# Kernel optimization log

Measured on AMD Instinct MI355X. Metric: run time of the kernel, lower is better.

The kernel has to match this reference:

```python
import jax, jax.numpy as jnp
import numpy as np

N, E, ND, ED, HID = 50000, 400000, 128, 64, 128
GIN = 2 * ND + 2  # gnn1 input dim
CIN = 2 * HID + ED  # classifier input dim


def seg_mean(v, idx, n):
    s = jax.ops.segment_sum(v, idx, num_segments=n)
    cnt = jax.ops.segment_sum(jnp.ones((v.shape[0], 1), v.dtype), idx, num_segments=n)
    return s / jnp.maximum(cnt, 1.0)


def layer_norm(h, g, b):
    mu = h.mean(-1, keepdims=True)
    var = ((h - mu) ** 2).mean(-1, keepdims=True)
    return (h - mu) / jnp.sqrt(var + 1e-5) * g + b


def gatv2(h, src, dst, ea, wl, wr, we, att, bias, n, heads):
    # PyG GATv2Conv, concat=False, negative_slope=0.2, add_self_loops with fill_value='mean'
    C = wl.shape[1] // heads
    loop_attr = seg_mean(ea, dst, n)  # self-loop edge_attr = mean of incoming edge_attr
    ar = jnp.arange(n, dtype=src.dtype)
    s = jnp.concatenate([src, ar])
    d = jnp.concatenate([dst, ar])
    ea2 = jnp.concatenate([ea, loop_attr], axis=0)
    xl = (h @ wl).reshape(n, heads, C)
    xr = (h @ wr).reshape(n, heads, C)
    e = xl[s] + xr[d] + (ea2 @ we).reshape(-1, heads, C)  # [E2, H, C]
    e = jax.nn.leaky_relu(e, 0.2)
    logit = (e * att).sum(-1)  # [E2, H]
    m = jax.ops.segment_max(logit, d, num_segments=n)
    m = jnp.where(jnp.isfinite(m), m, 0.0)
    a = jnp.exp(logit - m[d])
    denom = jax.ops.segment_sum(a, d, num_segments=n)
    a = a / jnp.maximum(denom[d], 1e-16)
    out = jax.ops.segment_sum(xl[s] * a[..., None], d, num_segments=n)  # [N, H, C]
    return out.mean(axis=1) + bias


def setup_inputs() -> dict:
    key = jax.random.key(0)
    ks = jax.random.split(key, 32)
    w = lambda k, sh: jax.random.normal(k, sh, jnp.float32) * 0.05
    x = jax.random.normal(ks[0], (N, ND), jnp.float32)
    node_stats = jax.random.uniform(ks[1], (N, 2), jnp.float32)
    src = jax.random.randint(ks[2], (E,), 0, N)
    dst = (src + 1 + jax.random.randint(ks[3], (E,), 0, N - 1)) % N  # guarantees src != dst
    edge_index = jnp.stack([src, dst]).astype(jnp.int32)
    edge_attr = jax.random.normal(ks[4], (E, ED), jnp.float32)
    return {
        'x': x, 'node_stats': node_stats, 'edge_index': edge_index, 'edge_attr': edge_attr,
        'epw': w(ks[5], (ED, ND)), 'epb': jnp.zeros((ND,), jnp.float32),
        'g1wl': w(ks[6], (GIN, 2 * HID)), 'g1wr': w(ks[7], (GIN, 2 * HID)),
        'g1we': w(ks[8], (ED, 2 * HID)), 'g1att': w(ks[9], (2, HID)), 'g1b': jnp.zeros((HID,), jnp.float32),
        'n1g': jnp.ones((HID,), jnp.float32), 'n1b': jnp.zeros((HID,), jnp.float32),
        'g2wl': w(ks[10], (HID, HID)), 'g2wr': w(ks[11], (HID, HID)),
        'g2we': w(ks[12], (ED, HID)), 'g2att': w(ks[13], (1, HID)), 'g2b': jnp.zeros((HID,), jnp.float32),
        'n2g': jnp.ones((HID,), jnp.float32), 'n2b': jnp.zeros((HID,), jnp.float32),
        'c1w': w(ks[14], (CIN, HID)), 'c1b': jnp.zeros((HID,), jnp.float32),
        'c2w': w(ks[15], (HID, HID // 2)), 'c2b': jnp.zeros((HID // 2,), jnp.float32),
        'c3w': w(ks[16], (HID // 2, 1)), 'c3b': jnp.zeros((1,), jnp.float32),
    }


def reference(x, node_stats, edge_index, edge_attr, epw, epb, g1wl, g1wr, g1we, g1att, g1b,
              n1g, n1b, g2wl, g2wr, g2we, g2att, g2b, n2g, n2b, c1w, c1b, c2w, c2b, c3w, c3b):
    src, dst = edge_index[0], edge_index[1]
    n = x.shape[0]
    emb = jax.nn.relu(edge_attr @ epw + epb)  # [E, ND]
    x_out = seg_mean(emb, src, n)
    x_in = seg_mean(emb, dst, n)
    xi = jnp.concatenate([x_out, x_in, node_stats], axis=1)  # [N, GIN]
    h1 = jax.nn.elu(layer_norm(gatv2(xi, src, dst, edge_attr, g1wl, g1wr, g1we, g1att, g1b, n, 2), n1g, n1b))
    h2 = jax.nn.elu(layer_norm(gatv2(h1, src, dst, edge_attr, g2wl, g2wr, g2we, g2att, g2b, n, 1), n2g, n2b))
    er = jnp.concatenate([h2[src], h2[dst], edge_attr], axis=1)  # [E, CIN]
    h = jax.nn.relu(er @ c1w + c1b)
    h = jax.nn.relu(h @ c2w + c2b)
    return h @ c3w + c3b  # [E, 1]
```

## Files before the change

kernel.cpp:

```cpp
#include <hip/hip_runtime.h>
#include <cstdint>
#include <cstddef>


static inline int cdiv(int a, int b) { return (a + b - 1) / b; }

typedef __attribute__((ext_vector_type(8))) short bfrag;
typedef __attribute__((ext_vector_type(4))) float ffrag;

__device__ __forceinline__ float bf2f(unsigned short u) {
  return __uint_as_float(((unsigned)u) << 16);
}
__device__ __forceinline__ unsigned short f2bf(float f) {
  unsigned b = __float_as_uint(f);
  return (unsigned short)((b + 0x7FFFu + ((b >> 16) & 1u)) >> 16);
}

struct PrepJobs {
  const float* src[11];
  unsigned short* dst[11];
  int K[11], Nc[11], KC[11], ld[11];
};
__global__ void prep_bt(PrepJobs J) {
  int j = blockIdx.x;
  int K = J.K[j], Nc = J.Nc[j], KC = J.KC[j], ld = J.ld[j];
  const float* S = J.src[j];
  unsigned short* D = J.dst[j];
  for (int n = blockIdx.y; n < Nc; n += gridDim.y)
    for (int t = threadIdx.x; t < KC; t += blockDim.x) {
      float v = (t < K) ? S[(size_t)t * ld + n] : 0.f;
      D[(size_t)n * KC + t] = f2bf(v);
    }
}

__global__ __launch_bounds__(256) void cvt_bf16(const float* __restrict__ in,
                                                unsigned short* __restrict__ out,
                                                int n4) {
  for (int i = blockIdx.x * blockDim.x + threadIdx.x; i < n4;
       i += gridDim.x * blockDim.x) {
    float4 v = ((const float4*)in)[i];
    ((ushort4*)out)[i] = make_ushort4(f2bf(v.x), f2bf(v.y), f2bf(v.z), f2bf(v.w));
  }
}

__global__ void count_deg(const int* __restrict__ src, const int* __restrict__ dst,
                          int* __restrict__ dsrc, int* __restrict__ ddst, int E) {
  int t = blockIdx.x * blockDim.x + threadIdx.x;
  if (t < E) {
    atomicAdd(&dsrc[src[t]], 1);
    atomicAdd(&ddst[dst[t]], 1);
  }
}

__global__ __launch_bounds__(256) void scan_local(
    const int* __restrict__ degA, const int* __restrict__ degB,
    int* __restrict__ rowA, int* __restrict__ rowB, int* __restrict__ bsum,
    int N, int nb) {
  __shared__ int s[256];
  int arr = blockIdx.y;
  const int* deg = arr ? degB : degA;
  int* row = arr ? rowB : rowA;
  int b = blockIdx.x;
  int i = b * 256 + threadIdx.x;
  int v = (i < N) ? deg[i] : 0;
  s[threadIdx.x] = v;
  __syncthreads();
  for (int off = 1; off < 256; off <<= 1) {
    int t = (threadIdx.x >= off) ? s[threadIdx.x - off] : 0;
    __syncthreads();
    s[threadIdx.x] += t;
    __syncthreads();
  }
  int incl = s[threadIdx.x];
  if (i < N) row[i] = incl - v;
  if (threadIdx.x == 255) bsum[arr * nb + b] = incl;
}

__global__ __launch_bounds__(1024) void scan_bsums(int* __restrict__ bsum, int nb,
                                                   int* __restrict__ rowA,
                                                   int* __restrict__ rowB, int N) {
  __shared__ int s[1024];
  int tid = threadIdx.x;
  for (int arr = 0; arr < 2; arr++) {
    int v = (tid < nb) ? bsum[arr * nb + tid] : 0;
    s[tid] = v;
    __syncthreads();
    for (int off = 1; off < 1024; off <<= 1) {
      int t = (tid >= off) ? s[tid - off] : 0;
      __syncthreads();
      s[tid] += t;
      __syncthreads();
    }
    if (tid < nb) bsum[arr * nb + tid] = s[tid] - v;
    if (tid == nb - 1) {
      int* row = arr ? rowB : rowA;
      row[N] = s[tid];
    }
    __syncthreads();
  }
}

__global__ void scan_add(int* __restrict__ rowA, int* __restrict__ rowB,
                         int* __restrict__ curA, const int* __restrict__ bsum,
                         int N, int nb) {
  int arr = blockIdx.y;
  int* row = arr ? rowB : rowA;
  int b = blockIdx.x;
  int i = b * 256 + threadIdx.x;
  if (i < N) {
    int v = row[i] + bsum[arr * nb + b];
    row[i] = v;
    if (arr == 0) curA[i] = v;
  }
}

__global__ void ext_fix(const int* __restrict__ row_dst, int* __restrict__ row_ext,
                        int* __restrict__ cur_ext, int* __restrict__ ext_eid,
                        int E, int N) {
  int i = blockIdx.x * blockDim.x + threadIdx.x;
  if (i <= N) row_ext[i] = row_dst[i] + i;
  if (i < N) {
    cur_ext[i] = row_dst[i] + i;
    ext_eid[row_dst[i + 1] + i] = E + i;
  }
}

__global__ void scatter_eid(const int* __restrict__ src, const int* __restrict__ dst,
                            int* __restrict__ csrc, int* __restrict__ cext,
                            int* __restrict__ esrc, int* __restrict__ ext_eid,
                            int E) {
  int t = blockIdx.x * blockDim.x + threadIdx.x;
  if (t < E) {
    int p = atomicAdd(&csrc[src[t]], 1);
    esrc[p] = t;
    int q = atomicAdd(&cext[dst[t]], 1);
    ext_eid[q] = t;
  }
}

struct ASrc {
  const float *p0, *p1, *p2;
  int ld0, ld1, ld2, k0, k1;
};
__device__ __forceinline__ float loadA(const ASrc& a, int m, int k) {
  if (k < a.k0) return a.p0[(size_t)m * a.ld0 + k];
  if (k < a.k1) return a.p1[(size_t)m * a.ld1 + (k - a.k0)];
  return a.p2[(size_t)m * a.ld2 + (k - a.k1)];
}
__device__ __forceinline__ int regionOf(const ASrc& a, int k) {
  return k < a.k0 ? 0 : (k < a.k1 ? 1 : 2);
}

template <int ABF>
__device__ __forceinline__ void stageA(
    const ASrc& A, const unsigned short* __restrict__ Abf, int lda,
    unsigned short* asb, int m0, int kc, int M, int K, int tid) {
  int row = tid & 63, kq = tid >> 6;
  int gm = m0 + row;
  if (ABF) {
    const unsigned short* rp = Abf + (size_t)gm * lda + kc + kq * 16;
    ushort4 z = make_ushort4(0, 0, 0, 0);
#pragma unroll
    for (int q = 0; q < 4; q++) {
      ushort4 v = (gm < M) ? *(const ushort4*)(rp + q * 4) : z;
      *(ushort4*)&asb[row * 72 + kq * 16 + q * 4] = v;
    }
  } else {
    bool fastc = (kc + 64 <= K) && (regionOf(A, kc) == regionOf(A, kc + 63)) &&
                 (gm < M);
    if (fastc) {
      int r = regionOf(A, kc);
      const float* p;
      int ld, koff;
      if (r == 0) { p = A.p0; ld = A.ld0; koff = 0; }
      else if (r == 1) { p = A.p1; ld = A.ld1; koff = A.k0; }
      else { p = A.p2; ld = A.ld2; koff = A.k1; }
      const float* rp = p + (size_t)gm * ld + (kc - koff) + kq * 16;
#pragma unroll
      for (int q = 0; q < 4; q++) {
        float4 v = *(const float4*)(rp + q * 4);
        *(ushort4*)&asb[row * 72 + kq * 16 + q * 4] =
            make_ushort4(f2bf(v.x), f2bf(v.y), f2bf(v.z), f2bf(v.w));
      }
    } else {
#pragma unroll
      for (int q = 0; q < 16; q++) {
        int kk = kc + kq * 16 + q;
        float v = (gm < M && kk < K) ? loadA(A, gm, kk) : 0.f;
        asb[row * 72 + kq * 16 + q] = f2bf(v);
      }
    }
  }
}

template <int ACT, int OBF, int ABF>
__global__ __launch_bounds__(256) void gemm_mfma(
    ASrc A, const unsigned short* __restrict__ Abf, int lda,
    const unsigned short* __restrict__ Bt, int ldbt,
    const float* __restrict__ bias, void* __restrict__ Cv, int ldc, int M, int K) {
  __shared__ __align__(16) unsigned short asb[64 * 72];
  __shared__ __align__(16) unsigned short bsb[128 * 72];
  int tid = threadIdx.x;
  int m0 = blockIdx.x * 64, n0 = blockIdx.y * 128;
  int lane = tid & 63, wave = tid >> 6;
  int quad = lane >> 4, l16 = lane & 15;
  ffrag zero = {0.f, 0.f, 0.f, 0.f};
  ffrag acc[8];
#pragma unroll
  for (int t = 0; t < 8; t++) acc[t] = zero;
  int KC = (K + 63) & ~63;
  for (int kc = 0; kc < KC; kc += 64) {
    __syncthreads();
    stageA<ABF>(A, Abf, lda, asb, m0, kc, M, K, tid);
    {
      int n = tid >> 1, hf = tid & 1;
      const ushort4* rp = (const ushort4*)(Bt + (size_t)(n0 + n) * ldbt + kc + hf * 32);
      ushort4* dp = (ushort4*)&bsb[n * 72 + hf * 32];
#pragma unroll
      for (int i = 0; i < 8; i++) dp[i] = rp[i];
    }
    __syncthreads();
    int arow = wave * 16 + l16;
    bfrag a0 = *(const bfrag*)&asb[arow * 72 + quad * 8];
    bfrag a1 = *(const bfrag*)&asb[arow * 72 + 32 + quad * 8];
#pragma unroll
    for (int t = 0; t < 8; t++) {
      int bn = t * 16 + l16;
      bfrag b0 = *(const bfrag*)&bsb[bn * 72 + quad * 8];
      bfrag b1 = *(const bfrag*)&bsb[bn * 72 + 32 + quad * 8];
      acc[t] = __builtin_amdgcn_mfma_f32_16x16x32_bf16(a0, b0, acc[t], 0, 0, 0);
      acc[t] = __builtin_amdgcn_mfma_f32_16x16x32_bf16(a1, b1, acc[t], 0, 0, 0);
    }
  }
#pragma unroll
  for (int t = 0; t < 8; t++) {
    int col = n0 + t * 16 + l16;
    float bv = bias ? bias[col] : 0.f;
#pragma unroll
    for (int r = 0; r < 4; r++) {
      int row = m0 + wave * 16 + quad * 4 + r;
      if (row < M) {
        float v = acc[t][r] + bv;
        if (ACT == 1) v = fmaxf(v, 0.f);
        if (OBF)
          ((unsigned short*)Cv)[(size_t)row * ldc + col] = f2bf(v);
        else
          ((float*)Cv)[(size_t)row * ldc + col] = v;
      }
    }
  }
}

template <int OBF, int ABF>
__global__ __launch_bounds__(256) void gemm_dual(
    ASrc A, const unsigned short* __restrict__ Abf, int lda,
    const unsigned short* __restrict__ Bt1, const unsigned short* __restrict__ Bt2,
    int ldbt, void* __restrict__ Cv1, void* __restrict__ Cv2, int ldc,
    int M, int K) {
  __shared__ __align__(16) unsigned short asb[64 * 72];
  __shared__ __align__(16) unsigned short bsb[128 * 72];
  int tid = threadIdx.x;
  int m0 = blockIdx.x * 64, n0 = blockIdx.y * 128;
  int lane = tid & 63, wave = tid >> 6;
  int quad = lane >> 4, l16 = lane & 15;
  ffrag zero = {0.f, 0.f, 0.f, 0.f};
  ffrag acc1[8], acc2[8];
#pragma unroll
  for (int t = 0; t < 8; t++) { acc1[t] = zero; acc2[t] = zero; }
  int KC = (K + 63) & ~63;
  int arow = wave * 16 + l16;
  for (int kc = 0; kc < KC; kc += 64) {
    __syncthreads();
    stageA<ABF>(A, Abf, lda, asb, m0, kc, M, K, tid);
    {
      int n = tid >> 1, hf = tid & 1;
      const ushort4* rp = (const ushort4*)(Bt1 + (size_t)(n0 + n) * ldbt + kc + hf * 32);
      ushort4* dp = (ushort4*)&bsb[n * 72 + hf * 32];
#pragma unroll
      for (int i = 0; i < 8; i++) dp[i] = rp[i];
    }
    __syncthreads();
    bfrag a0 = *(const bfrag*)&asb[arow * 72 + quad * 8];
    bfrag a1 = *(const bfrag*)&asb[arow * 72 + 32 + quad * 8];
#pragma unroll
    for (int t = 0; t < 8; t++) {
      int bn = t * 16 + l16;
      bfrag b0 = *(const bfrag*)&bsb[bn * 72 + quad * 8];
      bfrag b1 = *(const bfrag*)&bsb[bn * 72 + 32 + quad * 8];
      acc1[t] = __builtin_amdgcn_mfma_f32_16x16x32_bf16(a0, b0, acc1[t], 0, 0, 0);
      acc1[t] = __builtin_amdgcn_mfma_f32_16x16x32_bf16(a1, b1, acc1[t], 0, 0, 0);
    }
    __syncthreads();
    {
      int n = tid >> 1, hf = tid & 1;
      const ushort4* rp = (const ushort4*)(Bt2 + (size_t)(n0 + n) * ldbt + kc + hf * 32);
      ushort4* dp = (ushort4*)&bsb[n * 72 + hf * 32];
#pragma unroll
      for (int i = 0; i < 8; i++) dp[i] = rp[i];
    }
    __syncthreads();
#pragma unroll
    for (int t = 0; t < 8; t++) {
      int bn = t * 16 + l16;
      bfrag b0 = *(const bfrag*)&bsb[bn * 72 + quad * 8];
      bfrag b1 = *(const bfrag*)&bsb[bn * 72 + 32 + quad * 8];
      acc2[t] = __builtin_amdgcn_mfma_f32_16x16x32_bf16(a0, b0, acc2[t], 0, 0, 0);
      acc2[t] = __builtin_amdgcn_mfma_f32_16x16x32_bf16(a1, b1, acc2[t], 0, 0, 0);
    }
  }
#pragma unroll
  for (int t = 0; t < 8; t++) {
    int col = n0 + t * 16 + l16;
#pragma unroll
    for (int r = 0; r < 4; r++) {
      int row = m0 + wave * 16 + quad * 4 + r;
      if (row < M) {
        if (OBF) {
          ((unsigned short*)Cv1)[(size_t)row * ldc + col] = f2bf(acc1[t][r]);
          ((unsigned short*)Cv2)[(size_t)row * ldc + col] = f2bf(acc2[t][r]);
        } else {
          ((float*)Cv1)[(size_t)row * ldc + col] = acc1[t][r];
          ((float*)Cv2)[(size_t)row * ldc + col] = acc2[t][r];
        }
      }
    }
  }
}

__global__ __launch_bounds__(256) void gather_mean(
    const int* __restrict__ row_src, const int* __restrict__ eid_src,
    const int* __restrict__ row_ext, const int* __restrict__ ext_eid,
    const unsigned short* __restrict__ emb, const unsigned short* __restrict__ eab,
    float* __restrict__ xout, float* __restrict__ xin,
    unsigned short* __restrict__ lattrb, int N) {
  int lane = threadIdx.x & 63, wid = threadIdx.x >> 6;
  int n = blockIdx.x * 4 + wid;
  int side = blockIdx.y;
  if (n >= N) return;
  int lo, hi;
  const int* eid;
  if (side) { lo = row_ext[n]; hi = row_ext[n + 1] - 1; eid = ext_eid; }
  else { lo = row_src[n]; hi = row_src[n + 1]; eid = eid_src; }
  int half = lane >> 5;
  int l32 = lane & 31;
  int c4 = l32 * 4;
  float a0 = 0.f, a1 = 0.f, a2 = 0.f, a3 = 0.f;
  float la0 = 0.f, la1 = 0.f;
  int j = lo;
  for (; j + 1 < hi; j += 2) {
    int e = eid[j + half];
    ushort4 v = *(const ushort4*)&emb[(size_t)e * 128 + c4];
    a0 += bf2f(v.x); a1 += bf2f(v.y); a2 += bf2f(v.z); a3 += bf2f(v.w);
    if (side) {
      ushort2 u = *(const ushort2*)&eab[(size_t)e * 64 + l32 * 2];
      la0 += bf2f(u.x); la1 += bf2f(u.y);
    }
  }
  if (j < hi && half == 0) {
    int e = eid[j];
    ushort4 v = *(const ushort4*)&emb[(size_t)e * 128 + c4];
    a0 += bf2f(v.x); a1 += bf2f(v.y); a2 += bf2f(v.z); a3 += bf2f(v.w);
    if (side) {
      ushort2 u = *(const ushort2*)&eab[(size_t)e * 64 + l32 * 2];
      la0 += bf2f(u.x); la1 += bf2f(u.y);
    }
  }
  a0 += __shfl_xor(a0, 32);
  a1 += __shfl_xor(a1, 32);
  a2 += __shfl_xor(a2, 32);
  a3 += __shfl_xor(a3, 32);
  if (side) {
    la0 += __shfl_xor(la0, 32);
    la1 += __shfl_xor(la1, 32);
  }
  float r = 1.f / fmaxf((float)(hi - lo), 1.f);
  if (half == 0) {
    float* ob = side ? xin : xout;
    *(float4*)&ob[(size_t)n * 128 + c4] =
        make_float4(a0 * r, a1 * r, a2 * r, a3 * r);
    if (side)
      *(ushort2*)&lattrb[(size_t)n * 64 + l32 * 2] =
          make_ushort2(f2bf(la0 * r), f2bf(la1 * r));
  }
}

template <int H>
__global__ __launch_bounds__(256) void attn_logits_mfma(
    const unsigned short* __restrict__ xl, const unsigned short* __restrict__ xr,
    const int* __restrict__ src, const int* __restrict__ dst,
    const unsigned short* __restrict__ eab, const unsigned short* __restrict__ lattrb,
    const int* __restrict__ ext_eid,
    const unsigned short* __restrict__ wet, const float* __restrict__ att,
    float* __restrict__ lg, int E, int N) {
  constexpr int HC = H * 128;
  __shared__ __align__(16) unsigned short asb[64 * 72];
  __shared__ __align__(16) unsigned short bsb[128 * 72];
  __shared__ float atts[128];
  __shared__ int sidx[64], didx[64];
  unsigned short* Cs = bsb;
  int tid = threadIdx.x;
  int E2 = E + N;
  int i0 = blockIdx.x * 64;
  int lane = tid & 63, wave = tid >> 6, quad = lane >> 4, l16 = lane & 15;
  if (tid < 64) {
    int j = i0 + tid;
    int s = 0, d = 0;
    if (j < E2) {
      int e = ext_eid[j];
      if (e < E) { s = src[e]; d = dst[e]; }
      else { s = d = e - E; }
    }
    sidx[tid] = s;
    didx[tid] = d;
  }
  {
    int row = tid & 63, kq = tid >> 6;
    int j = i0 + row;
    if (j < E2) {
      int e = ext_eid[j];
      const unsigned short* ap =
          (e < E) ? eab + (size_t)e * 64 : lattrb + (size_t)(e - E) * 64;
      const ushort4* rp = (const ushort4*)(ap + kq * 16);
#pragma unroll
      for (int q = 0; q < 4; q++)
        *(ushort4*)&asb[row * 72 + kq * 16 + q * 4] = rp[q];
    } else {
      ushort4 z = make_ushort4(0, 0, 0, 0);
#pragma unroll
      for (int q = 0; q < 4; q++) *(ushort4*)&asb[row * 72 + kq * 16 + q * 4] = z;
    }
  }
  int er = tid >> 4, cc = tid & 15;
  ffrag zero = {0.f, 0.f, 0.f, 0.f};
  for (int head = 0; head < H; head++) {
    int n0 = head * 128;
    __syncthreads();
    if (tid < 128) atts[tid] = att[n0 + tid];
    {
      int n = tid >> 1, hf = tid & 1;
      const ushort4* rp = (const ushort4*)(wet + (size_t)(n0 + n) * 64 + hf * 32);
      ushort4* dp = (ushort4*)&bsb[n * 72 + hf * 32];
#pragma unroll
      for (int i = 0; i < 8; i++) dp[i] = rp[i];
    }
    __syncthreads();
    int arow = wave * 16 + l16;
    bfrag a0 = *(const bfrag*)&asb[arow * 72 + quad * 8];
    bfrag a1 = *(const bfrag*)&asb[arow * 72 + 32 + quad * 8];
    ffrag acc[8];
#pragma unroll
    for (int t = 0; t < 8; t++) {
      acc[t] = zero;
      int bn = t * 16 + l16;
      bfrag b0 = *(const bfrag*)&bsb[bn * 72 + quad * 8];
      bfrag b1 = *(const bfrag*)&bsb[bn * 72 + 32 + quad * 8];
      acc[t] = __builtin_amdgcn_mfma_f32_16x16x32_bf16(a0, b0, acc[t], 0, 0, 0);
      acc[t] = __builtin_amdgcn_mfma_f32_16x16x32_bf16(a1, b1, acc[t], 0, 0, 0);
    }
    __syncthreads();
    {
      int rb = wave * 16 + quad * 4;
#pragma unroll
      for (int t = 0; t < 8; t++)
#pragma unroll
        for (int r = 0; r < 4; r++)
          Cs[(rb + r) * 136 + t * 16 + l16] = f2bf(acc[t][r]);
    }
    __syncthreads();
#pragma unroll
    for (int i2 = 0; i2 < 4; i2++) {
      int r = er * 4 + i2;
      int gi = i0 + r;
      float ps = 0.f;
      if (gi < E2) {
        int s = sidx[r], d = didx[r];
#pragma unroll
        for (int h = 0; h < 2; h++) {
          int c = h * 64 + cc * 4;
          ushort4 mv = *(const ushort4*)&Cs[r * 136 + c];
          ushort4 xlu = *(const ushort4*)&xl[(size_t)s * HC + n0 + c];
          ushort4 xru = *(const ushort4*)&xr[(size_t)d * HC + n0 + c];
          float e0 = bf2f(mv.x) + bf2f(xlu.x) + bf2f(xru.x);
          float e1 = bf2f(mv.y) + bf2f(xlu.y) + bf2f(xru.y);
          float e2 = bf2f(mv.z) + bf2f(xlu.z) + bf2f(xru.z);
          float e3 = bf2f(mv.w) + bf2f(xlu.w) + bf2f(xru.w);
          e0 = e0 > 0.f ? e0 : 0.2f * e0;
          e1 = e1 > 0.f ? e1 : 0.2f * e1;
          e2 = e2 > 0.f ? e2 : 0.2f * e2;
          e3 = e3 > 0.f ? e3 : 0.2f * e3;
          ps += e0 * atts[c + 0] + e1 * atts[c + 1] + e2 * atts[c + 2] +
                e3 * atts[c + 3];
        }
      }
      ps += __shfl_xor(ps, 1);
      ps += __shfl_xor(ps, 2);
      ps += __shfl_xor(ps, 4);
      ps += __shfl_xor(ps, 8);
      if (cc == 0 && gi < E2) lg[(size_t)gi * H + head] = ps;
    }
  }
}

template <int H>
__global__ __launch_bounds__(256) void attn_fused(
    const unsigned short* __restrict__ xl, const float* __restrict__ lg,
    const int* __restrict__ row_ext, const int* __restrict__ ext_eid,
    const int* __restrict__ src, const float* __restrict__ bias,
    const float* __restrict__ gam, const float* __restrict__ bet,
    unsigned short* __restrict__ hout, int E, int N) {
  constexpr int HC = H * 128;
  constexpr int CPL = HC / 64;
  int lane = threadIdx.x & 63, wid = threadIdx.x >> 6;
  int n = blockIdx.x * 4 + wid;
  if (n >= N) return;
  int lo = row_ext[n], hi = row_ext[n + 1];
  int myh = (H == 2) ? (lane >> 5) : 0;
  int colbase = (H == 2) ? (myh * 128 + (lane & 31) * 4) : (lane * 2);
  float asum = 0.f;
  float acc[CPL] = {};
  for (int j = lo; j < hi; j++) {
    int e = ext_eid[j];
    int s = (e < E) ? src[e] : (e - E);
    float a = __expf(fminf(lg[(size_t)j * H + myh], 60.f));
    asum += a;
    const unsigned short* xp = &xl[(size_t)s * HC + colbase];
    if (H == 2) {
      ushort4 u = *(const ushort4*)xp;
      acc[0] += a * bf2f(u.x);
      acc[1] += a * bf2f(u.y);
      acc[2] += a * bf2f(u.z);
      acc[3] += a * bf2f(u.w);
    } else {
      ushort2 u = *(const ushort2*)xp;
      acc[0] += a * bf2f(u.x);
      acc[1] += a * bf2f(u.y);
    }
  }
  float inv = 1.f / fmaxf(asum, 1e-16f);
#pragma unroll
  for (int k = 0; k < CPL; k++) acc[k] *= inv;
  int ch;
  if (H == 2) {
#pragma unroll
    for (int k = 0; k < CPL; k++) acc[k] = (acc[k] + __shfl_xor(acc[k], 32)) * 0.5f;
    ch = (lane & 31) * CPL;
  } else {
    ch = lane * CPL;
  }
#pragma unroll
  for (int k = 0; k < CPL; k++) acc[k] += bias[ch + k];
  float s = 0.f;
#pragma unroll
  for (int k = 0; k < CPL; k++) s += acc[k];
#pragma unroll
  for (int mm = 1; mm < 64; mm <<= 1) s += __shfl_xor(s, mm);
  constexpr float dupn = (H == 2) ? 256.f : 128.f;
  float mu = s / dupn;
  float vs = 0.f;
#pragma unroll
  for (int k = 0; k < CPL; k++) {
    acc[k] -= mu;
    vs += acc[k] * acc[k];
  }
#pragma unroll
  for (int mm = 1; mm < 64; mm <<= 1) vs += __shfl_xor(vs, mm);
  float rstd = rsqrtf(vs / dupn + 1e-5f);
  float y[CPL];
#pragma unroll
  for (int k = 0; k < CPL; k++) {
    float v = acc[k] * rstd * gam[ch + k] + bet[ch + k];
    y[k] = v > 0.f ? v : expm1f(v);
  }
  if (H == 2) {
    if (lane < 32)
      *(ushort4*)&hout[(size_t)n * 128 + ch] =
          make_ushort4(f2bf(y[0]), f2bf(y[1]), f2bf(y[2]), f2bf(y[3]));
  } else {
    *(ushort2*)&hout[(size_t)n * 128 + ch] = make_ushort2(f2bf(y[0]), f2bf(y[1]));
  }
}

__global__ __launch_bounds__(256) void classifier_mfma(
    const unsigned short* __restrict__ eab, const unsigned short* __restrict__ Wct,
    const int* __restrict__ eid_src,
    const int* __restrict__ src, const int* __restrict__ dst,
    const float* __restrict__ P, const float* __restrict__ Q,
    const float* __restrict__ c1b, const unsigned short* __restrict__ c2t,
    const float* __restrict__ c2b, const float* __restrict__ c3w,
    const float* __restrict__ c3b, float* __restrict__ out, int E) {
  __shared__ __align__(16) unsigned short asb[64 * 72];
  __shared__ __align__(16) unsigned short bsb[128 * 72];
  __shared__ __align__(16) unsigned short t1s[64 * 136];
  __shared__ float c1bs[128];
  __shared__ float c2bs[64], c3ws[64];
  __shared__ int sidx[64], didx[64], eidx[64];
  int tid = threadIdx.x;
  int e0 = blockIdx.x * 64;
  int lane = tid & 63, wave = tid >> 6, quad = lane >> 4, l16 = lane & 15;
  if (tid < 128) c1bs[tid] = c1b[tid];
  if (tid < 64) {
    c2bs[tid] = c2b[tid];
    c3ws[tid] = c3w[tid];
    int j = e0 + tid;
    int e = (j < E) ? eid_src[j] : 0;
    eidx[tid] = (j < E) ? e : -1;
    sidx[tid] = src[e];
    didx[tid] = dst[e];
  }
  {
    int row = tid & 63, kq = tid >> 6;
    int j = e0 + row;
    if (j < E) {
      int e = eid_src[j];
      const ushort4* rp = (const ushort4*)(eab + (size_t)e * 64 + kq * 16);
#pragma unroll
      for (int q = 0; q < 4; q++)
        *(ushort4*)&asb[row * 72 + kq * 16 + q * 4] = rp[q];
    } else {
      ushort4 z = make_ushort4(0, 0, 0, 0);
#pragma unroll
      for (int q = 0; q < 4; q++) *(ushort4*)&asb[row * 72 + kq * 16 + q * 4] = z;
    }
  }
  {
    int n = tid >> 1, hf = tid & 1;
    const ushort4* rp = (const ushort4*)(Wct + (size_t)n * 64 + hf * 32);
    ushort4* dp = (ushort4*)&bsb[n * 72 + hf * 32];
#pragma unroll
    for (int i = 0; i < 8; i++) dp[i] = rp[i];
  }
  __syncthreads();
  ffrag zero = {0.f, 0.f, 0.f, 0.f};
  int arow = wave * 16 + l16;
  {
    bfrag a0 = *(const bfrag*)&asb[arow * 72 + quad * 8];
    bfrag a1 = *(const bfrag*)&asb[arow * 72 + 32 + quad * 8];
    ffrag acc[8];
#pragma unroll
    for (int t = 0; t < 8; t++) {
      acc[t] = zero;
      int bn = t * 16 + l16;
      bfrag b0 = *(const bfrag*)&bsb[bn * 72 + quad * 8];
      bfrag b1 = *(const bfrag*)&bsb[bn * 72 + 32 + quad * 8];
      acc[t] = __builtin_amdgcn_mfma_f32_16x16x32_bf16(a0, b0, acc[t], 0, 0, 0);
      acc[t] = __builtin_amdgcn_mfma_f32_16x16x32_bf16(a1, b1, acc[t], 0, 0, 0);
    }
    __syncthreads();
    int rb = wave * 16 + quad * 4;
#pragma unroll
    for (int t = 0; t < 8; t++)
#pragma unroll
      for (int r = 0; r < 4; r++)
        t1s[(rb + r) * 136 + t * 16 + l16] = f2bf(acc[t][r]);
  }
  __syncthreads();
  {
    int erow = tid >> 4, ccc = tid & 15;
#pragma unroll
    for (int i2 = 0; i2 < 4; i2++) {
      int r = erow * 4 + i2;
      int s = sidx[r], d = didx[r];
#pragma unroll
      for (int h = 0; h < 2; h++) {
        int c = h * 64 + ccc * 4;
        ushort4 mv = *(const ushort4*)&t1s[r * 136 + c];
        float4 pv = *(const float4*)&P[(size_t)s * 128 + c];
        float4 qv = *(const float4*)&Q[(size_t)d * 128 + c];
        float v0 = fmaxf(bf2f(mv.x) + pv.x + qv.x + c1bs[c + 0], 0.f);
        float v1 = fmaxf(bf2f(mv.y) + pv.y + qv.y + c1bs[c + 1], 0.f);
        float v2 = fmaxf(bf2f(mv.z) + pv.z + qv.z + c1bs[c + 2], 0.f);
        float v3 = fmaxf(bf2f(mv.w) + pv.w + qv.w + c1bs[c + 3], 0.f);
        *(ushort4*)&t1s[r * 136 + c] =
            make_ushort4(f2bf(v0), f2bf(v1), f2bf(v2), f2bf(v3));
      }
    }
    int n = tid >> 2, qq = tid & 3;
    const ushort4* rp = (const ushort4*)(c2t + (size_t)n * 128 + qq * 32);
    ushort4* dp = (ushort4*)&bsb[n * 136 + qq * 32];
#pragma unroll
    for (int i = 0; i < 8; i++) dp[i] = rp[i];
  }
  __syncthreads();
  {
    bfrag pa[4];
#pragma unroll
    for (int kc = 0; kc < 4; kc++)
      pa[kc] = *(const bfrag*)&t1s[arow * 136 + kc * 32 + quad * 8];
    ffrag acc2[4];
#pragma unroll
    for (int t = 0; t < 4; t++) {
      acc2[t] = zero;
      int bn = t * 16 + l16;
#pragma unroll
      for (int kc = 0; kc < 4; kc++) {
        bfrag b = *(const bfrag*)&bsb[bn * 136 + kc * 32 + quad * 8];
        acc2[t] = __builtin_amdgcn_mfma_f32_16x16x32_bf16(pa[kc], b, acc2[t], 0, 0, 0);
      }
    }
    float c3b0 = c3b[0];
    float rsum[4] = {0.f, 0.f, 0.f, 0.f};
#pragma unroll
    for (int t = 0; t < 4; t++) {
      int col = t * 16 + l16;
      float cb = c2bs[col], cw = c3ws[col];
#pragma unroll
      for (int r = 0; r < 4; r++)
        rsum[r] += fmaxf(acc2[t][r] + cb, 0.f) * cw;
    }
#pragma unroll
    for (int r = 0; r < 4; r++) {
      rsum[r] += __shfl_xor(rsum[r], 1);
      rsum[r] += __shfl_xor(rsum[r], 2);
      rsum[r] += __shfl_xor(rsum[r], 4);
      rsum[r] += __shfl_xor(rsum[r], 8);
    }
    if (l16 == 0) {
#pragma unroll
      for (int r = 0; r < 4; r++) {
        int e = eidx[wave * 16 + quad * 4 + r];
        if (e >= 0) out[e] = rsum[r] + c3b0;
      }
    }
  }
}

extern "C" void kernel_launch(void* const* d_in, const int* in_sizes, int n_in,
                              void* d_out, int out_size, void* d_ws, size_t ws_size,
                              hipStream_t stream) {
  const int N = in_sizes[1] / 2;
  const int E = in_sizes[3] / 64;
  const int E2 = E + N;
  const int nb = cdiv(N, 256);

  const float* node_stats = (const float*)d_in[1];
  const int* src = (const int*)d_in[2];
  const int* dst = (const int*)d_in[2] + E;
  const float* edge_attr = (const float*)d_in[3];
  const float* epw = (const float*)d_in[4];
  const float* epb = (const float*)d_in[5];
  const float* g1wl = (const float*)d_in[6];
  const float* g1wr = (const float*)d_in[7];
  const float* g1we = (const float*)d_in[8];
  const float* g1att = (const float*)d_in[9];
  const float* g1b = (const float*)d_in[10];
  const float* n1g = (const float*)d_in[11];
  const float* n1b = (const float*)d_in[12];
  const float* g2wl = (const float*)d_in[13];
  const float* g2wr = (const float*)d_in[14];
  const float* g2we = (const float*)d_in[15];
  const float* g2att = (const float*)d_in[16];
  const float* g2b = (const float*)d_in[17];
  const float* n2g = (const float*)d_in[18];
  const float* n2b = (const float*)d_in[19];
  const float* c1w = (const float*)d_in[20];
  const float* c1b = (const float*)d_in[21];
  const float* c2w = (const float*)d_in[22];
  const float* c2b = (const float*)d_in[23];
  const float* c3w = (const float*)d_in[24];
  const float* c3b = (const float*)d_in[25];
  float* out = (float*)d_out;

  float* w = (float*)d_ws;
  size_t o = 0;
  auto alloc = [&](size_t n) { float* p = w + o; o += n; return p; };
  float* xout = alloc((size_t)N * 128);
  float* xin = alloc((size_t)N * 128);
  float* lattr = alloc((size_t)N * 64);
  float* lg = alloc((size_t)E2 * 2);
  int* row_src = (int*)alloc((size_t)(N + 1));
  int* row_dst = (int*)alloc((size_t)(N + 1));
  int* row_ext = (int*)alloc((size_t)(N + 1));
  int* deg_src = (int*)alloc((size_t)N);
  int* deg_dst = (int*)alloc((size_t)N);
  int* cur_src = (int*)alloc((size_t)N);
  int* cur_ext = (int*)alloc((size_t)N);
  int* eid_src = (int*)alloc((size_t)E);
  int* ext_eid = (int*)alloc((size_t)E2);
  int* bsum = (int*)alloc((size_t)2 * 1024);
  unsigned short* wb = (unsigned short*)alloc(140000);
  unsigned short* eab = (unsigned short*)alloc((size_t)E * 32);
  float* R = alloc((size_t)E * 64);
  unsigned short* Ru = (unsigned short*)R;
  unsigned short* emb = Ru;
  unsigned short* xl1b = Ru;
  unsigned short* xr1b = Ru + (size_t)N * 256;
  unsigned short* h1b = Ru + (size_t)N * 512;
  unsigned short* xl2b = Ru + (size_t)N * 640;
  unsigned short* xr2b = Ru + (size_t)N * 768;
  unsigned short* h2b = Ru + (size_t)N * 896;
  unsigned short* lattrb = (unsigned short*)lattr;
  float* P = xout;
  float* Q = xin;

  unsigned short* epwt = wb + 0;
  unsigned short* g1wlt = wb + 8192;
  unsigned short* g1wrt = wb + 90112;
  unsigned short* g1wet = wb + 172032;
  unsigned short* g2wlt = wb + 188416;
  unsigned short* g2wrt = wb + 204800;
  unsigned short* g2wet = wb + 221184;
  unsigned short* c1wat = wb + 229376;
  unsigned short* c1wbt = wb + 245760;
  unsigned short* c1wct = wb + 262144;
  unsigned short* c2t = wb + 270336;

  cvt_bf16<<<2048, 256, 0, stream>>>(edge_attr, eab, E * 16);
  PrepJobs J;
  auto setj = [&](int i, const float* s, unsigned short* d2, int K, int Nc,
                  int KC, int ld) {
    J.src[i] = s; J.dst[i] = d2; J.K[i] = K; J.Nc[i] = Nc; J.KC[i] = KC; J.ld[i] = ld;
  };
  setj(0, epw, epwt, 64, 128, 64, 128);
  setj(1, g1wl, g1wlt, 258, 256, 320, 256);
  setj(2, g1wr, g1wrt, 258, 256, 320, 256);
  setj(3, g1we, g1wet, 64, 256, 64, 256);
  setj(4, g2wl, g2wlt, 128, 128, 128, 128);
  setj(5, g2wr, g2wrt, 128, 128, 128, 128);
  setj(6, g2we, g2wet, 64, 128, 64, 128);
  setj(7, c1w, c1wat, 128, 128, 128, 128);
  setj(8, c1w + 128 * 128, c1wbt, 128, 128, 128, 128);
  setj(9, c1w + 256 * 128, c1wct, 64, 128, 64, 128);
  setj(10, c2w, c2t, 128, 64, 128, 64);
  prep_bt<<<dim3(11, 32), 256, 0, stream>>>(J);

  hipMemsetAsync(deg_src, 0, (size_t)2 * N * sizeof(int), stream);
  count_deg<<<cdiv(E, 256), 256, 0, stream>>>(src, dst, deg_src, deg_dst, E);
  scan_local<<<dim3(nb, 2), 256, 0, stream>>>(deg_src, deg_dst, row_src, row_dst,
                                              bsum, N, nb);
  scan_bsums<<<1, 1024, 0, stream>>>(bsum, nb, row_src, row_dst, N);
  scan_add<<<dim3(nb, 2), 256, 0, stream>>>(row_src, row_dst, cur_src, bsum, N, nb);
  ext_fix<<<cdiv(N + 1, 256), 256, 0, stream>>>(row_dst, row_ext, cur_ext,
                                                ext_eid, E, N);
  scatter_eid<<<cdiv(E, 256), 256, 0, stream>>>(src, dst, cur_src, cur_ext,
                                                eid_src, ext_eid, E);

  ASrc dummy{nullptr, nullptr, nullptr, 0, 0, 0, 0, 0};

  gemm_mfma<1, 1, 1><<<dim3(cdiv(E, 64), 1), 256, 0, stream>>>(
      dummy, eab, 64, epwt, 64, epb, emb, 128, E, 64);
  gather_mean<<<dim3(cdiv(N, 4), 2), 256, 0, stream>>>(
      row_src, eid_src, row_ext, ext_eid, emb, eab, xout, xin, lattrb, N);

  {
    ASrc a{xout, xin, node_stats, 128, 128, 2, 128, 256};
    dim3 g(cdiv(N, 64), 2);
    gemm_dual<1, 0><<<g, 256, 0, stream>>>(a, nullptr, 0, g1wlt, g1wrt, 320,
                                           xl1b, xr1b, 256, N, 258);
  }

  attn_logits_mfma<2><<<cdiv(E2, 64), 256, 0, stream>>>(
      xl1b, xr1b, src, dst, eab, lattrb, ext_eid, g1wet, g1att, lg, E, N);
  attn_fused<2><<<cdiv(N, 4), 256, 0, stream>>>(xl1b, lg, row_ext, ext_eid, src,
                                                g1b, n1g, n1b, h1b, E, N);

  {
    dim3 g(cdiv(N, 64), 1);
    gemm_dual<1, 1><<<g, 256, 0, stream>>>(dummy, h1b, 128, g2wlt, g2wrt, 128,
                                           xl2b, xr2b, 128, N, 128);
  }

  attn_logits_mfma<1><<<cdiv(E2, 64), 256, 0, stream>>>(
      xl2b, xr2b, src, dst, eab, lattrb, ext_eid, g2wet, g2att, lg, E, N);
  attn_fused<1><<<cdiv(N, 4), 256, 0, stream>>>(xl2b, lg, row_ext, ext_eid, src,
                                                g2b, n2g, n2b, h2b, E, N);

  {
    dim3 g(cdiv(N, 64), 1);
    gemm_dual<0, 1><<<g, 256, 0, stream>>>(dummy, h2b, 128, c1wat, c1wbt, 128,
                                           P, Q, 128, N, 128);
  }
  classifier_mfma<<<cdiv(E, 64), 256, 0, stream>>>(
      eab, c1wct, eid_src, src, dst, P, Q, c1b, c2t, c2b, c3w, c3b, out, E);
}
```

Before: 946.7 us.

## Materialize sorted src/dst, precompute exp logits, fuse classifier first layer on edges

The edge scatter now also writes the source and destination node of each dst-sorted extended edge, so the attention kernels read ssrc/sdst directly instead of going through ext_eid and src/dst. The exp of each clamped logit moves into the logits kernel, which stores attention weights instead of raw logits. The separate node-level GEMM that produced P/Q for the classifier is removed. The classifier instead gathers bf16 h2 rows per edge and runs the h2[src]/h2[dst] products with MFMA inside the edge kernel. This saves a kernel launch and the fp32 P/Q traffic, at the cost of about four times more matrix work per edge, extra LDS staging and barriers, and two more int arrays written during preprocessing.

```diff
diff --git a/kernel.cpp b/kernel.cpp
--- a/kernel.cpp
+++ b/kernel.cpp
@@ -116,25 +116,33 @@
 
 __global__ void ext_fix(const int* __restrict__ row_dst, int* __restrict__ row_ext,
                         int* __restrict__ cur_ext, int* __restrict__ ext_eid,
+                        int* __restrict__ ssrc, int* __restrict__ sdst,
                         int E, int N) {
   int i = blockIdx.x * blockDim.x + threadIdx.x;
   if (i <= N) row_ext[i] = row_dst[i] + i;
   if (i < N) {
     cur_ext[i] = row_dst[i] + i;
-    ext_eid[row_dst[i + 1] + i] = E + i;
+    int p = row_dst[i + 1] + i;
+    ext_eid[p] = E + i;
+    ssrc[p] = i;
+    sdst[p] = i;
   }
 }
 
 __global__ void scatter_eid(const int* __restrict__ src, const int* __restrict__ dst,
                             int* __restrict__ csrc, int* __restrict__ cext,
                             int* __restrict__ esrc, int* __restrict__ ext_eid,
+                            int* __restrict__ ssrc, int* __restrict__ sdst,
                             int E) {
   int t = blockIdx.x * blockDim.x + threadIdx.x;
   if (t < E) {
-    int p = atomicAdd(&csrc[src[t]], 1);
+    int s = src[t], d = dst[t];
+    int p = atomicAdd(&csrc[s], 1);
     esrc[p] = t;
-    int q = atomicAdd(&cext[dst[t]], 1);
+    int q = atomicAdd(&cext[d], 1);
     ext_eid[q] = t;
+    ssrc[q] = s;
+    sdst[q] = d;
   }
 }
 
@@ -387,7 +395,7 @@
 template <int H>
 __global__ __launch_bounds__(256) void attn_logits_mfma(
     const unsigned short* __restrict__ xl, const unsigned short* __restrict__ xr,
-    const int* __restrict__ src, const int* __restrict__ dst,
+    const int* __restrict__ ssrc, const int* __restrict__ sdst,
     const unsigned short* __restrict__ eab, const unsigned short* __restrict__ lattrb,
     const int* __restrict__ ext_eid,
     const unsigned short* __restrict__ wet, const float* __restrict__ att,
@@ -404,14 +412,8 @@
   int lane = tid & 63, wave = tid >> 6, quad = lane >> 4, l16 = lane & 15;
   if (tid < 64) {
     int j = i0 + tid;
-    int s = 0, d = 0;
-    if (j < E2) {
-      int e = ext_eid[j];
-      if (e < E) { s = src[e]; d = dst[e]; }
-      else { s = d = e - E; }
-    }
-    sidx[tid] = s;
-    didx[tid] = d;
+    sidx[tid] = (j < E2) ? ssrc[j] : 0;
+    didx[tid] = (j < E2) ? sdst[j] : 0;
   }
   {
     int row = tid & 63, kq = tid >> 6;
@@ -496,7 +498,8 @@
       ps += __shfl_xor(ps, 2);
       ps += __shfl_xor(ps, 4);
       ps += __shfl_xor(ps, 8);
-      if (cc == 0 && gi < E2) lg[(size_t)gi * H + head] = ps;
+      if (cc == 0 && gi < E2)
+        lg[(size_t)gi * H + head] = __expf(fminf(ps, 60.f));
     }
   }
 }
@@ -504,8 +507,8 @@
 template <int H>
 __global__ __launch_bounds__(256) void attn_fused(
     const unsigned short* __restrict__ xl, const float* __restrict__ lg,
-    const int* __restrict__ row_ext, const int* __restrict__ ext_eid,
-    const int* __restrict__ src, const float* __restrict__ bias,
+    const int* __restrict__ row_ext, const int* __restrict__ ssrc,
+    const float* __restrict__ bias,
     const float* __restrict__ gam, const float* __restrict__ bet,
     unsigned short* __restrict__ hout, int E, int N) {
   constexpr int HC = H * 128;
@@ -519,9 +522,8 @@
   float asum = 0.f;
   float acc[CPL] = {};
   for (int j = lo; j < hi; j++) {
-    int e = ext_eid[j];
-    int s = (e < E) ? src[e] : (e - E);
-    float a = __expf(fminf(lg[(size_t)j * H + myh], 60.f));
+    int s = ssrc[j];
+    float a = lg[(size_t)j * H + myh];
     asum += a;
     const unsigned short* xp = &xl[(size_t)s * HC + colbase];
     if (H == 2) {
@@ -581,10 +583,11 @@
 }
 
 __global__ __launch_bounds__(256) void classifier_mfma(
-    const unsigned short* __restrict__ eab, const unsigned short* __restrict__ Wct,
+    const unsigned short* __restrict__ eab, const unsigned short* __restrict__ h2b,
     const int* __restrict__ eid_src,
     const int* __restrict__ src, const int* __restrict__ dst,
-    const float* __restrict__ P, const float* __restrict__ Q,
+    const unsigned short* __restrict__ c1wct, const unsigned short* __restrict__ c1wat,
+    const unsigned short* __restrict__ c1wbt,
     const float* __restrict__ c1b, const unsigned short* __restrict__ c2t,
     const float* __restrict__ c2b, const float* __restrict__ c3w,
     const float* __restrict__ c3b, float* __restrict__ out, int E) {
@@ -602,11 +605,16 @@
     c2bs[tid] = c2b[tid];
     c3ws[tid] = c3w[tid];
     int j = e0 + tid;
-    int e = (j < E) ? eid_src[j] : 0;
-    eidx[tid] = (j < E) ? e : -1;
-    sidx[tid] = src[e];
-    didx[tid] = dst[e];
-  }
+    int e = (j < E) ? eid_src[j] : -1;
+    eidx[tid] = e;
+    sidx[tid] = (e >= 0) ? src[e] : 0;
+    didx[tid] = (e >= 0) ? dst[e] : 0;
+  }
+  ffrag zero = {0.f, 0.f, 0.f, 0.f};
+  ffrag acc[8];
+#pragma unroll
+  for (int t = 0; t < 8; t++) acc[t] = zero;
+  int arow = wave * 16 + l16;
   {
     int row = tid & 63, kq = tid >> 6;
     int j = e0 + row;
@@ -621,57 +629,69 @@
 #pragma unroll
       for (int q = 0; q < 4; q++) *(ushort4*)&asb[row * 72 + kq * 16 + q * 4] = z;
     }
-  }
-  {
     int n = tid >> 1, hf = tid & 1;
-    const ushort4* rp = (const ushort4*)(Wct + (size_t)n * 64 + hf * 32);
+    const ushort4* rp2 = (const ushort4*)(c1wct + (size_t)n * 64 + hf * 32);
     ushort4* dp = (ushort4*)&bsb[n * 72 + hf * 32];
 #pragma unroll
-    for (int i = 0; i < 8; i++) dp[i] = rp[i];
+    for (int i = 0; i < 8; i++) dp[i] = rp2[i];
   }
   __syncthreads();
-  ffrag zero = {0.f, 0.f, 0.f, 0.f};
-  int arow = wave * 16 + l16;
   {
     bfrag a0 = *(const bfrag*)&asb[arow * 72 + quad * 8];
     bfrag a1 = *(const bfrag*)&asb[arow * 72 + 32 + quad * 8];
-    ffrag acc[8];
 #pragma unroll
     for (int t = 0; t < 8; t++) {
-      acc[t] = zero;
       int bn = t * 16 + l16;
       bfrag b0 = *(const bfrag*)&bsb[bn * 72 + quad * 8];
       bfrag b1 = *(const bfrag*)&bsb[bn * 72 + 32 + quad * 8];
       acc[t] = __builtin_amdgcn_mfma_f32_16x16x32_bf16(a0, b0, acc[t], 0, 0, 0);
       acc[t] = __builtin_amdgcn_mfma_f32_16x16x32_bf16(a1, b1, acc[t], 0, 0, 0);
     }
-    __syncthreads();
-    int rb = wave * 16 + quad * 4;
-#pragma unroll
-    for (int t = 0; t < 8; t++)
-#pragma unroll
-      for (int r = 0; r < 4; r++)
-        t1s[(rb + r) * 136 + t * 16 + l16] = f2bf(acc[t][r]);
+  }
+  for (int ph = 0; ph < 2; ph++) {
+    const int* idx = ph ? didx : sidx;
+    const unsigned short* Wt = ph ? c1wbt : c1wat;
+#pragma unroll
+    for (int kc = 0; kc < 2; kc++) {
+      __syncthreads();
+      {
+        int row = tid & 63, kq = tid >> 6;
+        int s = idx[row];
+        const ushort4* rp =
+            (const ushort4*)(h2b + (size_t)s * 128 + kc * 64 + kq * 16);
+#pragma unroll
+        for (int q = 0; q < 4; q++)
+          *(ushort4*)&asb[row * 72 + kq * 16 + q * 4] = rp[q];
+        int n = tid >> 1, hf = tid & 1;
+        const ushort4* rp2 =
+            (const ushort4*)(Wt + (size_t)n * 128 + kc * 64 + hf * 32);
+        ushort4* dp = (ushort4*)&bsb[n * 72 + hf * 32];
+#pragma unroll
+        for (int i = 0; i < 8; i++) dp[i] = rp2[i];
+      }
+      __syncthreads();
+      bfrag a0 = *(const bfrag*)&asb[arow * 72 + quad * 8];
+      bfrag a1 = *(const bfrag*)&asb[arow * 72 + 32 + quad * 8];
+#pragma unroll
+      for (int t = 0; t < 8; t++) {
+        int bn = t * 16 + l16;
+        bfrag b0 = *(const bfrag*)&bsb[bn * 72 + quad * 8];
+        bfrag b1 = *(const bfrag*)&bsb[bn * 72 + 32 + quad * 8];
+        acc[t] = __builtin_amdgcn_mfma_f32_16x16x32_bf16(a0, b0, acc[t], 0, 0, 0);
+        acc[t] = __builtin_amdgcn_mfma_f32_16x16x32_bf16(a1, b1, acc[t], 0, 0, 0);
+      }
+    }
   }
   __syncthreads();
   {
-    int erow = tid >> 4, ccc = tid & 15;
-#pragma unroll
-    for (int i2 = 0; i2 < 4; i2++) {
-      int r = erow * 4 + i2;
-      int s = sidx[r], d = didx[r];
-#pragma unroll
-      for (int h = 0; h < 2; h++) {
-        int c = h * 64 + ccc * 4;
-        ushort4 mv = *(const ushort4*)&t1s[r * 136 + c];
-        float4 pv = *(const float4*)&P[(size_t)s * 128 + c];
-        float4 qv = *(const float4*)&Q[(size_t)d * 128 + c];
-        float v0 = fmaxf(bf2f(mv.x) + pv.x + qv.x + c1bs[c + 0], 0.f);
-        float v1 = fmaxf(bf2f(mv.y) + pv.y + qv.y + c1bs[c + 1], 0.f);
-        float v2 = fmaxf(bf2f(mv.z) + pv.z + qv.z + c1bs[c + 2], 0.f);
-        float v3 = fmaxf(bf2f(mv.w) + pv.w + qv.w + c1bs[c + 3], 0.f);
-        *(ushort4*)&t1s[r * 136 + c] =
-            make_ushort4(f2bf(v0), f2bf(v1), f2bf(v2), f2bf(v3));
+    int rb = wave * 16 + quad * 4;
+#pragma unroll
+    for (int t = 0; t < 8; t++) {
+      int col = t * 16 + l16;
+#pragma unroll
+      for (int r = 0; r < 4; r++) {
+        float v = acc[t][r] + c1bs[col];
+        t1s[(rb + r) * 136 + col] = f2bf(fmaxf(v, 0.f));
       }
     }
     int n = tid >> 2, qq = tid & 3;
@@ -776,6 +796,8 @@
   int* cur_ext = (int*)alloc((size_t)N);
   int* eid_src = (int*)alloc((size_t)E);
   int* ext_eid = (int*)alloc((size_t)E2);
+  int* ssrc = (int*)alloc((size_t)E2);
+  int* sdst = (int*)alloc((size_t)E2);
   int* bsum = (int*)alloc((size_t)2 * 1024);
   unsigned short* wb = (unsigned short*)alloc(140000);
   unsigned short* eab = (unsigned short*)alloc((size_t)E * 32);
@@ -789,8 +811,6 @@
   unsigned short* xr2b = Ru + (size_t)N * 768;
   unsigned short* h2b = Ru + (size_t)N * 896;
   unsigned short* lattrb = (unsigned short*)lattr;
-  float* P = xout;
-  float* Q = xin;
 
   unsigned short* epwt = wb + 0;
   unsigned short* g1wlt = wb + 8192;
@@ -830,9 +850,9 @@
   scan_bsums<<<1, 1024, 0, stream>>>(bsum, nb, row_src, row_dst, N);
   scan_add<<<dim3(nb, 2), 256, 0, stream>>>(row_src, row_dst, cur_src, bsum, N, nb);
   ext_fix<<<cdiv(N + 1, 256), 256, 0, stream>>>(row_dst, row_ext, cur_ext,
-                                                ext_eid, E, N);
+                                                ext_eid, ssrc, sdst, E, N);
   scatter_eid<<<cdiv(E, 256), 256, 0, stream>>>(src, dst, cur_src, cur_ext,
-                                                eid_src, ext_eid, E);
+                                                eid_src, ext_eid, ssrc, sdst, E);
 
   ASrc dummy{nullptr, nullptr, nullptr, 0, 0, 0, 0, 0};
 
@@ -849,8 +869,8 @@
   }
 
   attn_logits_mfma<2><<<cdiv(E2, 64), 256, 0, stream>>>(
-      xl1b, xr1b, src, dst, eab, lattrb, ext_eid, g1wet, g1att, lg, E, N);
-  attn_fused<2><<<cdiv(N, 4), 256, 0, stream>>>(xl1b, lg, row_ext, ext_eid, src,
+      xl1b, xr1b, ssrc, sdst, eab, lattrb, ext_eid, g1wet, g1att, lg, E, N);
+  attn_fused<2><<<cdiv(N, 4), 256, 0, stream>>>(xl1b, lg, row_ext, ssrc,
                                                 g1b, n1g, n1b, h1b, E, N);
 
   {
@@ -860,15 +880,11 @@
   }
 
   attn_logits_mfma<1><<<cdiv(E2, 64), 256, 0, stream>>>(
-      xl2b, xr2b, src, dst, eab, lattrb, ext_eid, g2wet, g2att, lg, E, N);
-  attn_fused<1><<<cdiv(N, 4), 256, 0, stream>>>(xl2b, lg, row_ext, ext_eid, src,
+      xl2b, xr2b, ssrc, sdst, eab, lattrb, ext_eid, g2wet, g2att, lg, E, N);
+  attn_fused<1><<<cdiv(N, 4), 256, 0, stream>>>(xl2b, lg, row_ext, ssrc,
                                                 g2b, n2g, n2b, h2b, E, N);
 
-  {
-    dim3 g(cdiv(N, 64), 1);
-    gemm_dual<0, 1><<<g, 256, 0, stream>>>(dummy, h2b, 128, c1wat, c1wbt, 128,
-                                           P, Q, 128, N, 128);
-  }
   classifier_mfma<<<cdiv(E, 64), 256, 0, stream>>>(
-      eab, c1wct, eid_src, src, dst, P, Q, c1b, c2t, c2b, c3w, c3b, out, E);
-}
+      eab, h2b, eid_src, src, dst, c1wct, c1wat, c1wbt, c1b, c2t, c2b, c3w,
+      c3b, out, E);
+}
```

Measured after the change: 888.6 us. 6.1% less time.
